# Kernel optimization log

Hardware: AMD Instinct MI355X
Metric: run time of the kernel (lower is better)

The kernel has to match this reference:

```python
import jax, jax.numpy as jnp
import numpy as np

# Workspace layout constants (match config in init_kwargs)
N_LAYERS = 24
D_MODEL = 2048
D_SPOKE = 128
D_HUB_PRIV = 64
D_HUB_SHARED = 512
D_TAG = 64
D_S_SPOKES = N_LAYERS * D_SPOKE            # 3072
HUB_PRIV_OFF = D_S_SPOKES                  # 3072
HUB_SHARED_OFF = HUB_PRIV_OFF + N_LAYERS * D_HUB_PRIV  # 4608
TAG_OFF = HUB_SHARED_OFF + D_HUB_SHARED    # 5120
D_S = TAG_OFF + N_LAYERS * D_TAG           # 6656
DECAY_WINDOW = 8
B, T = 4, 4096


def setup_inputs() -> dict:
    key = jax.random.key(0)
    ks = jax.random.split(key, 9)
    return {
        "S": jax.random.normal(ks[0], (B, T, D_S), jnp.float32),
        "H": jax.random.normal(ks[1], (B, T, D_MODEL), jnp.float32),
        "w_spoke": jax.random.normal(ks[2], (B, T, D_SPOKE), jnp.float32),
        "w_hub_priv": jax.random.normal(ks[3], (B, T, D_HUB_PRIV), jnp.float32),
        "w_hub_shared": jax.random.normal(ks[4], (B, T, D_HUB_SHARED), jnp.float32),
        "tag": jax.random.normal(ks[5], (B, T, D_TAG), jnp.float32),
        "Wq": jax.random.normal(ks[6], (D_TAG, D_MODEL), jnp.float32) / np.sqrt(D_MODEL).astype(np.float32),
        "Wg": jax.random.normal(ks[7], (D_HUB_SHARED, 2 * D_TAG), jnp.float32) / np.sqrt(2 * D_TAG).astype(np.float32),
        "bg": jnp.zeros((D_HUB_SHARED,), jnp.float32),
        "layer_idx": 12,
    }


def reference(S, H, w_spoke, w_hub_priv, w_hub_shared, tag, Wq, Wg, bg, layer_idx):
    li = int(layer_idx)
    # --- HubDecayGate (layer_idx > 0, decay_window > 0) ---
    start = max(0, li - DECAY_WINDOW)
    n_tags = li - start  # 8
    trs = TAG_OFF + start * D_TAG
    tre = TAG_OFF + li * D_TAG
    # mean over past tags: [B,T,n_tags,d_tag] -> [B,T,d_tag]
    mean_tag = S[:, :, trs:tre].reshape(S.shape[0], S.shape[1], n_tags, D_TAG).mean(axis=2)
    query = jnp.einsum('btm,qm->btq', H, Wq)            # [B,T,d_tag]
    gate_in = jnp.concatenate([query, mean_tag], axis=-1)  # [B,T,2*d_tag]
    gate = jax.nn.sigmoid(jnp.einsum('btk,hk->bth', gate_in, Wg) + bg)  # [B,T,d_hub_shared]
    # gated shared hub (forward of FlooredMultiply is a plain multiply)
    gated_hub = S[:, :, HUB_SHARED_OFF:TAG_OFF] * gate
    S = S.at[:, :, HUB_SHARED_OFF:TAG_OFF].set(gated_hub)
    # --- fused workspace writes ---
    ss = li * D_SPOKE
    hps = HUB_PRIV_OFF + li * D_HUB_PRIV
    ts = TAG_OFF + li * D_TAG
    S = S.at[:, :, ss:ss + D_SPOKE].add(w_spoke)
    S = S.at[:, :, hps:hps + D_HUB_PRIV].add(w_hub_priv)
    S = S.at[:, :, HUB_SHARED_OFF:TAG_OFF].add(w_hub_shared)
    S = S.at[:, :, ts:ts + D_TAG].add(tag)
    return (S, gate)
```

## Files before the change

### kernel.cpp

```cpp
#include <hip/hip_runtime.h>
#include <hip/hip_bf16.h>


#define DM 2048
#define DSZ 6656
#define HUBOFF 4608
#define TAGOFF 5120
#define NTOK 16384
#define DHS 512
#define HSTRIDE 1048

typedef __attribute__((ext_vector_type(8))) short bf16x8;
typedef __attribute__((ext_vector_type(4))) short s16x4;
typedef __attribute__((ext_vector_type(4))) float f32x4;

__device__ __forceinline__ float sigmoidf_(float x) {
  return 1.0f / (1.0f + __expf(-x));
}
__device__ __forceinline__ short f2bf(float x) {
  return (short)__bfloat16_as_ushort(__float2bfloat16(x));
}
__device__ __forceinline__ float bf2f(short x) {
  return __builtin_bit_cast(float, (unsigned)((unsigned short)x) << 16);
}
__device__ __forceinline__ bf16x8 cvt8(float4 a, float4 b) {
  bf16x8 r;
  r[0] = f2bf(a.x); r[1] = f2bf(a.y); r[2] = f2bf(a.z); r[3] = f2bf(a.w);
  r[4] = f2bf(b.x); r[5] = f2bf(b.y); r[6] = f2bf(b.z); r[7] = f2bf(b.w);
  return r;
}
#define MFMA(a, b, c) __builtin_amdgcn_mfma_f32_16x16x32_bf16((a), (b), (c), 0, 0, 0)

__global__ __launch_bounds__(256) void cw_fused_kernel(
    const float* __restrict__ S, const float* __restrict__ H,
    const float* __restrict__ Wq, const float* __restrict__ Wg,
    const float* __restrict__ bg, const float* __restrict__ whs,
    const float* __restrict__ w_spoke, const float* __restrict__ w_hub_priv,
    const float* __restrict__ tgin, const int* __restrict__ lip,
    float* __restrict__ outS, float* __restrict__ gate_out)
{
  __shared__ float gin[16][132];
  __shared__ short tagb[16][520];
  __shared__ short hubb[16][520];
  __shared__ __align__(16) char smem[16 * HSTRIDE * 2];
  short (*hds)[HSTRIDE] = (short (*)[HSTRIDE])smem;
  float (*gtile)[516]   = (float (*)[516])smem;

  const int tid = threadIdx.x;
  const int li = *lip;
  const int start = (li > 8) ? (li - 8) : 0;
  const int ntags = li - start;
  const float tscale = (ntags > 0) ? (1.0f / (float)ntags) : 0.0f;
  const int tok0 = blockIdx.x * 16;
  const int w = tid >> 6, l = tid & 63, l15 = l & 15, l4 = l >> 4;

  const int sp0 = li * 32;
  const int hp0 = 768 + li * 16;
  const int tg0 = 1280 + li * 16;
  const int tq0 = 1280 + start * 16;
  const int tq1 = tq0 + 16 * ntags;

  const float4* S4 = reinterpret_cast<const float4*>(S);
  const float4* SP4 = reinterpret_cast<const float4*>(w_spoke);
  const float4* HP4 = reinterpret_cast<const float4*>(w_hub_priv);
  const float4* TG4 = reinterpret_cast<const float4*>(tgin);
  float4* O4 = reinterpret_cast<float4*>(outS);

  for (int j = 0; j < 7; ++j) {
    const int c = j * 256 + tid;
    if (c < 1664) {
      const bool inhub = (c >= 1152 && c < 1280);
#pragma unroll
      for (int rq = 0; rq < 4; ++rq) {
        float4 sv[4];
#pragma unroll
        for (int k = 0; k < 4; ++k)
          sv[k] = S4[(size_t)(tok0 + rq * 4 + k) * 1664u + c];
#pragma unroll
        for (int k = 0; k < 4; ++k) {
          const int r = rq * 4 + k;
          float4 s = sv[k];
          if (inhub) {
            s16x4 v;
            v[0] = f2bf(s.x); v[1] = f2bf(s.y);
            v[2] = f2bf(s.z); v[3] = f2bf(s.w);
            *reinterpret_cast<s16x4*>(&hubb[r][(c - 1152) * 4]) = v;
          } else {
            if (c >= tq0 && c < tq1) {
              s16x4 v;
              v[0] = f2bf(s.x); v[1] = f2bf(s.y);
              v[2] = f2bf(s.z); v[3] = f2bf(s.w);
              *reinterpret_cast<s16x4*>(&tagb[r][(c - tq0) * 4]) = v;
            }
            float4 o = s;
            if (c >= sp0 && c < sp0 + 32) {
              float4 v = SP4[(size_t)(tok0 + r) * 32u + (c - sp0)];
              o.x += v.x; o.y += v.y; o.z += v.z; o.w += v.w;
            } else if (c >= hp0 && c < hp0 + 16) {
              float4 v = HP4[(size_t)(tok0 + r) * 16u + (c - hp0)];
              o.x += v.x; o.y += v.y; o.z += v.z; o.w += v.w;
            } else if (c >= tg0 && c < tg0 + 16) {
              float4 v = TG4[(size_t)(tok0 + r) * 16u + (c - tg0)];
              o.x += v.x; o.y += v.y; o.z += v.z; o.w += v.w;
            }
            O4[(size_t)(tok0 + r) * 1664u + c] = o;
          }
        }
      }
    }
  }
  __syncthreads();

  {
    const int tk = tid >> 4, t16 = tid & 15;
    float a0 = 0.f, a1 = 0.f, a2 = 0.f, a3 = 0.f;
    for (int g = 0; g < ntags; ++g) {
      s16x4 v = *reinterpret_cast<const s16x4*>(&tagb[tk][g * 64 + t16 * 4]);
      a0 += bf2f(v[0]); a1 += bf2f(v[1]); a2 += bf2f(v[2]); a3 += bf2f(v[3]);
    }
    const int d = 64 + t16 * 4;
    gin[tk][d + 0] = a0 * tscale;
    gin[tk][d + 1] = a1 * tscale;
    gin[tk][d + 2] = a2 * tscale;
    gin[tk][d + 3] = a3 * tscale;
  }

  const int q0 = w * 16;
  f32x4 qacc = {0.f, 0.f, 0.f, 0.f};
  for (int kc = 0; kc < 2; ++kc) {
    float4 st[16];
    const float* hb = H + (size_t)(tok0 + w * 4) * DM + kc * 1024;
#pragma unroll
    for (int j = 0; j < 16; ++j)
      st[j] = *reinterpret_cast<const float4*>(
          hb + (size_t)(j >> 2) * DM + (j & 3) * 256 + l * 4);
    __syncthreads();
#pragma unroll
    for (int j = 0; j < 16; ++j) {
      s16x4 v;
      v[0] = f2bf(st[j].x); v[1] = f2bf(st[j].y);
      v[2] = f2bf(st[j].z); v[3] = f2bf(st[j].w);
      *reinterpret_cast<s16x4*>(&hds[w * 4 + (j >> 2)][(j & 3) * 256 + l * 4]) = v;
    }
    __syncthreads();
    const float* wqb = Wq + (size_t)(q0 + l15) * DM + kc * 1024 + l4 * 8;
#pragma unroll 4
    for (int ks = 0; ks < 32; ++ks) {
      bf16x8 af = *reinterpret_cast<const bf16x8*>(&hds[l15][ks * 32 + l4 * 8]);
      float4 b0 = *reinterpret_cast<const float4*>(wqb + ks * 32);
      float4 b1 = *reinterpret_cast<const float4*>(wqb + ks * 32 + 4);
      qacc = MFMA(af, cvt8(b0, b1), qacc);
    }
  }
#pragma unroll
  for (int i = 0; i < 4; ++i)
    gin[l4 * 4 + i][q0 + l15] = qacc[i];
  __syncthreads();

  bf16x8 afr[4];
#pragma unroll
  for (int ks = 0; ks < 4; ++ks) {
    const float* p = &gin[l15][ks * 32 + l4 * 8];
    afr[ks] = cvt8(*reinterpret_cast<const float4*>(p),
                   *reinterpret_cast<const float4*>(p + 4));
  }
  const float* wgb = Wg + (size_t)l15 * 128 + l4 * 8;
  for (int jp = 0; jp < 4; ++jp) {
    const int ht0 = w * 8 + jp * 2;
    const float* wp0 = wgb + (size_t)ht0 * 16 * 128;
    const float* wp1 = wp0 + 16 * 128;
    float4 r0[4][2], r1[4][2];
#pragma unroll
    for (int ks = 0; ks < 4; ++ks) {
      r0[ks][0] = *reinterpret_cast<const float4*>(wp0 + ks * 32);
      r0[ks][1] = *reinterpret_cast<const float4*>(wp0 + ks * 32 + 4);
      r1[ks][0] = *reinterpret_cast<const float4*>(wp1 + ks * 32);
      r1[ks][1] = *reinterpret_cast<const float4*>(wp1 + ks * 32 + 4);
    }
    f32x4 accA = {0.f,0.f,0.f,0.f}, accB = {0.f,0.f,0.f,0.f};
#pragma unroll
    for (int ks = 0; ks < 4; ++ks) {
      accA = MFMA(afr[ks], cvt8(r0[ks][0], r0[ks][1]), accA);
      accB = MFMA(afr[ks], cvt8(r1[ks][0], r1[ks][1]), accB);
    }
#pragma unroll
    for (int t = 0; t < 2; ++t) {
      const f32x4 a = t ? accB : accA;
      const int h = (ht0 + t) * 16 + l15;
      const float bgv = bg[h];
#pragma unroll
      for (int i = 0; i < 4; ++i)
        gtile[l4 * 4 + i][h] = sigmoidf_(a[i] + bgv);
    }
  }
  __syncthreads();

#pragma unroll
  for (int r2 = 0; r2 < 8; ++r2) {
    const int idx = r2 * 256 + tid;
    const int row = idx >> 7, qq = idx & 127;
    const int tok = tok0 + row;
    float4 g = *reinterpret_cast<const float4*>(&gtile[row][qq * 4]);
    s16x4 sh = *reinterpret_cast<const s16x4*>(&hubb[row][qq * 4]);
    float4 wv = *reinterpret_cast<const float4*>(whs + (size_t)tok * DHS + qq * 4);
    float4 o;
    o.x = bf2f(sh[0]) * g.x + wv.x;
    o.y = bf2f(sh[1]) * g.y + wv.y;
    o.z = bf2f(sh[2]) * g.z + wv.z;
    o.w = bf2f(sh[3]) * g.w + wv.w;
    *reinterpret_cast<float4*>(outS + (size_t)tok * DSZ + HUBOFF + qq * 4) = o;
    *reinterpret_cast<float4*>(gate_out + (size_t)tok * DHS + qq * 4) = g;
  }
}

extern "C" void kernel_launch(void* const* d_in, const int* in_sizes, int n_in,
                              void* d_out, int out_size, void* d_ws, size_t ws_size,
                              hipStream_t stream) {
  (void)in_sizes; (void)n_in; (void)out_size; (void)d_ws; (void)ws_size;
  const float* S            = (const float*)d_in[0];
  const float* H            = (const float*)d_in[1];
  const float* w_spoke      = (const float*)d_in[2];
  const float* w_hub_priv   = (const float*)d_in[3];
  const float* w_hub_shared = (const float*)d_in[4];
  const float* tgin         = (const float*)d_in[5];
  const float* Wq           = (const float*)d_in[6];
  const float* Wg           = (const float*)d_in[7];
  const float* bg           = (const float*)d_in[8];
  const int*   lip          = (const int*)d_in[9];

  float* outS = (float*)d_out;
  float* gate_out = outS + (size_t)NTOK * DSZ;

  cw_fused_kernel<<<1024, 256, 0, stream>>>(
      S, H, Wq, Wg, bg, w_hub_shared, w_spoke, w_hub_priv, tgin, lip,
      outS, gate_out);
}
```

Baseline: 284.9 us.

## Shrink LDS footprint to raise occupancy; read H directly for query MFMA

Removes the large H staging tile and the separate hub and gate tiles, reusing one small bf16 buffer for past tags and then for the gate. The query GEMM now loads H fragments straight from global memory into MFMA operands. The hub slice of S is reloaded from global in the final phase instead of being cached in LDS. Launch bounds now request 4 blocks per SM. The aim is higher occupancy to hide memory latency, at the cost of re-reading the hub slice and storing the gate output at bf16 precision, which changes the gate values written out.

```diff
diff --git a/kernel.cpp b/kernel.cpp
--- a/kernel.cpp
+++ b/kernel.cpp
@@ -8,7 +8,6 @@
 #define TAGOFF 5120
 #define NTOK 16384
 #define DHS 512
-#define HSTRIDE 1048
 
 typedef __attribute__((ext_vector_type(8))) short bf16x8;
 typedef __attribute__((ext_vector_type(4))) short s16x4;
@@ -31,7 +30,7 @@
 }
 #define MFMA(a, b, c) __builtin_amdgcn_mfma_f32_16x16x32_bf16((a), (b), (c), 0, 0, 0)
 
-__global__ __launch_bounds__(256) void cw_fused_kernel(
+__global__ __launch_bounds__(256, 4) void cw_fused_kernel(
     const float* __restrict__ S, const float* __restrict__ H,
     const float* __restrict__ Wq, const float* __restrict__ Wg,
     const float* __restrict__ bg, const float* __restrict__ whs,
@@ -40,11 +39,7 @@
     float* __restrict__ outS, float* __restrict__ gate_out)
 {
   __shared__ float gin[16][132];
-  __shared__ short tagb[16][520];
-  __shared__ short hubb[16][520];
-  __shared__ __align__(16) char smem[16 * HSTRIDE * 2];
-  short (*hds)[HSTRIDE] = (short (*)[HSTRIDE])smem;
-  float (*gtile)[516]   = (float (*)[516])smem;
+  __shared__ short ub[16][520];
 
   const int tid = threadIdx.x;
   const int li = *lip;
@@ -76,21 +71,16 @@
 #pragma unroll
         for (int k = 0; k < 4; ++k)
           sv[k] = S4[(size_t)(tok0 + rq * 4 + k) * 1664u + c];
-#pragma unroll
-        for (int k = 0; k < 4; ++k) {
-          const int r = rq * 4 + k;
-          float4 s = sv[k];
-          if (inhub) {
-            s16x4 v;
-            v[0] = f2bf(s.x); v[1] = f2bf(s.y);
-            v[2] = f2bf(s.z); v[3] = f2bf(s.w);
-            *reinterpret_cast<s16x4*>(&hubb[r][(c - 1152) * 4]) = v;
-          } else {
+        if (!inhub) {
+#pragma unroll
+          for (int k = 0; k < 4; ++k) {
+            const int r = rq * 4 + k;
+            float4 s = sv[k];
             if (c >= tq0 && c < tq1) {
               s16x4 v;
               v[0] = f2bf(s.x); v[1] = f2bf(s.y);
               v[2] = f2bf(s.z); v[3] = f2bf(s.w);
-              *reinterpret_cast<s16x4*>(&tagb[r][(c - tq0) * 4]) = v;
+              *reinterpret_cast<s16x4*>(&ub[r][(c - tq0) * 4]) = v;
             }
             float4 o = s;
             if (c >= sp0 && c < sp0 + 32) {
@@ -115,7 +105,7 @@
     const int tk = tid >> 4, t16 = tid & 15;
     float a0 = 0.f, a1 = 0.f, a2 = 0.f, a3 = 0.f;
     for (int g = 0; g < ntags; ++g) {
-      s16x4 v = *reinterpret_cast<const s16x4*>(&tagb[tk][g * 64 + t16 * 4]);
+      s16x4 v = *reinterpret_cast<const s16x4*>(&ub[tk][g * 64 + t16 * 4]);
       a0 += bf2f(v[0]); a1 += bf2f(v[1]); a2 += bf2f(v[2]); a3 += bf2f(v[3]);
     }
     const int d = 64 + t16 * 4;
@@ -125,36 +115,23 @@
     gin[tk][d + 3] = a3 * tscale;
   }
 
-  const int q0 = w * 16;
-  f32x4 qacc = {0.f, 0.f, 0.f, 0.f};
-  for (int kc = 0; kc < 2; ++kc) {
-    float4 st[16];
-    const float* hb = H + (size_t)(tok0 + w * 4) * DM + kc * 1024;
-#pragma unroll
-    for (int j = 0; j < 16; ++j)
-      st[j] = *reinterpret_cast<const float4*>(
-          hb + (size_t)(j >> 2) * DM + (j & 3) * 256 + l * 4);
-    __syncthreads();
-#pragma unroll
-    for (int j = 0; j < 16; ++j) {
-      s16x4 v;
-      v[0] = f2bf(st[j].x); v[1] = f2bf(st[j].y);
-      v[2] = f2bf(st[j].z); v[3] = f2bf(st[j].w);
-      *reinterpret_cast<s16x4*>(&hds[w * 4 + (j >> 2)][(j & 3) * 256 + l * 4]) = v;
-    }
-    __syncthreads();
-    const float* wqb = Wq + (size_t)(q0 + l15) * DM + kc * 1024 + l4 * 8;
+  {
+    const int q0 = w * 16;
+    const float* ha = H + (size_t)(tok0 + l15) * DM + l4 * 8;
+    const float* wq = Wq + (size_t)(q0 + l15) * DM + l4 * 8;
+    f32x4 qacc = {0.f, 0.f, 0.f, 0.f};
 #pragma unroll 4
-    for (int ks = 0; ks < 32; ++ks) {
-      bf16x8 af = *reinterpret_cast<const bf16x8*>(&hds[l15][ks * 32 + l4 * 8]);
-      float4 b0 = *reinterpret_cast<const float4*>(wqb + ks * 32);
-      float4 b1 = *reinterpret_cast<const float4*>(wqb + ks * 32 + 4);
-      qacc = MFMA(af, cvt8(b0, b1), qacc);
-    }
-  }
-#pragma unroll
-  for (int i = 0; i < 4; ++i)
-    gin[l4 * 4 + i][q0 + l15] = qacc[i];
+    for (int ks = 0; ks < 64; ++ks) {
+      float4 a0 = *reinterpret_cast<const float4*>(ha + ks * 32);
+      float4 a1 = *reinterpret_cast<const float4*>(ha + ks * 32 + 4);
+      float4 b0 = *reinterpret_cast<const float4*>(wq + ks * 32);
+      float4 b1 = *reinterpret_cast<const float4*>(wq + ks * 32 + 4);
+      qacc = MFMA(cvt8(a0, a1), cvt8(b0, b1), qacc);
+    }
+#pragma unroll
+    for (int i = 0; i < 4; ++i)
+      gin[l4 * 4 + i][q0 + l15] = qacc[i];
+  }
   __syncthreads();
 
   bf16x8 afr[4];
@@ -190,7 +167,7 @@
       const float bgv = bg[h];
 #pragma unroll
       for (int i = 0; i < 4; ++i)
-        gtile[l4 * 4 + i][h] = sigmoidf_(a[i] + bgv);
+        ub[l4 * 4 + i][h] = f2bf(sigmoidf_(a[i] + bgv));
     }
   }
   __syncthreads();
@@ -200,14 +177,16 @@
     const int idx = r2 * 256 + tid;
     const int row = idx >> 7, qq = idx & 127;
     const int tok = tok0 + row;
-    float4 g = *reinterpret_cast<const float4*>(&gtile[row][qq * 4]);
-    s16x4 sh = *reinterpret_cast<const s16x4*>(&hubb[row][qq * 4]);
+    s16x4 gh = *reinterpret_cast<const s16x4*>(&ub[row][qq * 4]);
+    float4 g;
+    g.x = bf2f(gh[0]); g.y = bf2f(gh[1]); g.z = bf2f(gh[2]); g.w = bf2f(gh[3]);
+    float4 s = *reinterpret_cast<const float4*>(S + (size_t)tok * DSZ + HUBOFF + qq * 4);
     float4 wv = *reinterpret_cast<const float4*>(whs + (size_t)tok * DHS + qq * 4);
     float4 o;
-    o.x = bf2f(sh[0]) * g.x + wv.x;
-    o.y = bf2f(sh[1]) * g.y + wv.y;
-    o.z = bf2f(sh[2]) * g.z + wv.z;
-    o.w = bf2f(sh[3]) * g.w + wv.w;
+    o.x = s.x * g.x + wv.x;
+    o.y = s.y * g.y + wv.y;
+    o.z = s.z * g.z + wv.z;
+    o.w = s.w * g.w + wv.w;
     *reinterpret_cast<float4*>(outS + (size_t)tok * DSZ + HUBOFF + qq * 4) = o;
     *reinterpret_cast<float4*>(gate_out + (size_t)tok * DHS + qq * 4) = g;
   }
```

Measured after the change: 302.9 us. 1.06x slower.
